# Optimization experiments

Measured on AMD Instinct MI355X. Metric: run time of the kernel, lower is better.

Reference implementation:

```python
import jax, jax.numpy as jnp
import numpy as np

B, N, F, H, F_ = 4, 2048, 64, 4, 64


def setup_inputs() -> dict:
    key = jax.random.key(0)
    kx, ka, kw, ks, kn = jax.random.split(key, 5)
    X = jax.random.normal(kx, (B, N, F), dtype=jnp.float32)
    A = (jax.random.uniform(ka, (B, N, N)) < 0.05).astype(jnp.float32)
    A = jnp.maximum(A, jnp.eye(N, dtype=jnp.float32)[None])
    W = jax.random.normal(kw, (H, F, F_), dtype=jnp.float32) * 0.1
    a_self = jax.random.normal(ks, (H, F_), dtype=jnp.float32) * 0.1
    a_neigh = jax.random.normal(kn, (H, F_), dtype=jnp.float32) * 0.1
    return {"X": X, "A": A, "W": W, "a_self": a_self, "a_neigh": a_neigh}


def reference(X, A, W, a_self, a_neigh):
    # linear transform per head: [B,H,N,F_]
    lin = jnp.einsum('bnf,hfo->bhno', X, W)
    # additive attention scores
    s_self = jnp.einsum('bhno,ho->bhn', lin, a_self)[:, :, :, None]   # [B,H,N,1]
    s_neigh = jnp.einsum('bhno,ho->bhn', lin, a_neigh)[:, :, None, :]  # [B,H,1,N]
    dense = s_self + s_neigh                                           # [B,H,N,N]
    dense = jnp.where(dense >= 0, dense, 0.2 * dense)                  # LeakyReLU(0.2)
    BIG = jnp.float32(1e10)
    mask = jnp.exp(A * -BIG) * -BIG                                    # 0 where edge, -1e10 where no edge
    logits = dense + mask[:, None, :, :]
    attn = jax.nn.softmax(logits, axis=-1)
    # dropout is identity at inference (attn_dropout=0.0)
    feats = jnp.einsum('bhnm,bhmo->bhno', attn, lin)                   # [B,H,N,F_]
    feats = jax.nn.relu(feats)                                         # activation before concat
    b, h, n, f_ = feats.shape
    out = feats.transpose(0, 2, 1, 3).reshape(b, n, h * f_)            # concat heads
    return out
```

## Files before the change

kernel.cpp:

```cpp
#include <hip/hip_runtime.h>
#include <hip/hip_bf16.h>

#define BB 4
#define NN 2048
#define FF 64
#define HH 4
#define FO 64
#define CAP 256


__global__ __launch_bounds__(256) void BatchGraphAttention_84378927497895_kernel(
    const float* __restrict__ W, const float* __restrict__ a_self,
    const float* __restrict__ a_neigh, float* __restrict__ w_self,
    float* __restrict__ w_neigh) {
  int t = threadIdx.x;
  int h = t >> 6;
  const float* Wp = W + t * FO;
  const float* as = a_self + h * FO;
  const float* an = a_neigh + h * FO;
  float acc_s = 0.f, acc_n = 0.f;
#pragma unroll
  for (int o = 0; o < FO; ++o) {
    float w = Wp[o];
    acc_s += w * as[o];
    acc_n += w * an[o];
  }
  w_self[t] = acc_s;
  w_neigh[t] = acc_n;
}

__global__ __launch_bounds__(256) void BatchGraphAttention_84378927497895_kernel2(
    const float* __restrict__ X, const float* __restrict__ w_self,
    const float* __restrict__ w_neigh, float* __restrict__ s_self,
    float* __restrict__ s_neigh) {
  int bn = blockIdx.x;
  int t = threadIdx.x, h = t >> 6, f = t & 63;
  float x = X[(size_t)bn * FF + f];
  float vs = x * w_self[h * FF + f];
  float vn = x * w_neigh[h * FF + f];
#pragma unroll
  for (int off = 32; off > 0; off >>= 1) {
    vs += __shfl_down(vs, off, 64);
    vn += __shfl_down(vn, off, 64);
  }
  if (f == 0) {
    int b = bn >> 11, n = bn & (NN - 1);
    int bh = b * HH + h;
    s_self[bh * NN + n] = vs;
    s_neigh[bh * NN + n] = vn;
  }
}

__global__ __launch_bounds__(256) void BatchGraphAttention_84378927497895_kernel3(
    const float* __restrict__ A, const float* __restrict__ X,
    const float* __restrict__ W, const float* __restrict__ s_self,
    const float* __restrict__ s_neigh, float* __restrict__ out) {
  int bn = blockIdx.x;
  int b = bn >> 11;
  int n = bn & (NN - 1);
  __shared__ unsigned short idx[CAP];
  __shared__ float plt[CAP][4];
  __shared__ float red[4][HH][FF];
  __shared__ float ys[HH][FF];
  __shared__ float sinv[HH];
  __shared__ int cnt_s;
  int t = threadIdx.x;
  int lane = t & 63, wv = t >> 6;
  if (t == 0) cnt_s = 0;
  __syncthreads();

  {
    const float4* Ar4 = (const float4*)(A + (size_t)bn * NN);
#pragma unroll
    for (int it = 0; it < 2; ++it) {
      int q = t + it * 256;
      float4 v = Ar4[q];
      unsigned base = (unsigned)q * 4u;
      if (v.x != 0.f) { int p = atomicAdd(&cnt_s, 1); if (p < CAP) idx[p] = (unsigned short)(base + 0); }
      if (v.y != 0.f) { int p = atomicAdd(&cnt_s, 1); if (p < CAP) idx[p] = (unsigned short)(base + 1); }
      if (v.z != 0.f) { int p = atomicAdd(&cnt_s, 1); if (p < CAP) idx[p] = (unsigned short)(base + 2); }
      if (v.w != 0.f) { int p = atomicAdd(&cnt_s, 1); if (p < CAP) idx[p] = (unsigned short)(base + 3); }
    }
  }
  __syncthreads();
  int cnt = cnt_s;
  if (cnt > CAP) cnt = CAP;

  {
    int h = wv;
    int bh = b * HH + h;
    float ss = s_self[bh * NN + n];
    const float* snp = s_neigh + (size_t)bh * NN;

    float lmax = -1e30f;
    for (int j = lane; j < cnt; j += 64) {
      float lg = ss + snp[idx[j]];
      lg = (lg >= 0.f) ? lg : 0.2f * lg;
      plt[j][h] = lg;
      lmax = fmaxf(lmax, lg);
    }
#pragma unroll
    for (int off = 32; off > 0; off >>= 1)
      lmax = fmaxf(lmax, __shfl_xor(lmax, off, 64));

    float lsum = 0.f;
    for (int j = lane; j < cnt; j += 64) {
      float e = __expf(plt[j][h] - lmax);
      plt[j][h] = e;
      lsum += e;
    }
#pragma unroll
    for (int off = 32; off > 0; off >>= 1) lsum += __shfl_xor(lsum, off, 64);
    if (lane == 0) sinv[h] = 1.f / lsum;
  }
  __syncthreads();

  {
    const float* xp = X + (size_t)b * NN * FF + lane;
    float y0 = 0.f, y1 = 0.f, y2 = 0.f, y3 = 0.f;
    int j = wv;
    for (; j + 12 < cnt; j += 16) {
      int m0 = idx[j], m1 = idx[j + 4], m2 = idx[j + 8], m3 = idx[j + 12];
      float4 p0 = *(const float4*)plt[j];
      float4 p1 = *(const float4*)plt[j + 4];
      float4 p2 = *(const float4*)plt[j + 8];
      float4 p3 = *(const float4*)plt[j + 12];
      float x0 = xp[m0 * FF];
      float x1 = xp[m1 * FF];
      float x2 = xp[m2 * FF];
      float x3 = xp[m3 * FF];
      y0 += p0.x * x0; y1 += p0.y * x0; y2 += p0.z * x0; y3 += p0.w * x0;
      y0 += p1.x * x1; y1 += p1.y * x1; y2 += p1.z * x1; y3 += p1.w * x1;
      y0 += p2.x * x2; y1 += p2.y * x2; y2 += p2.z * x2; y3 += p2.w * x2;
      y0 += p3.x * x3; y1 += p3.y * x3; y2 += p3.z * x3; y3 += p3.w * x3;
    }
    for (; j < cnt; j += 4) {
      float4 p = *(const float4*)plt[j];
      float x = xp[idx[j] * FF];
      y0 += p.x * x; y1 += p.y * x; y2 += p.z * x; y3 += p.w * x;
    }
    red[wv][0][lane] = y0;
    red[wv][1][lane] = y1;
    red[wv][2][lane] = y2;
    red[wv][3][lane] = y3;
  }
  __syncthreads();

  {
    int h = wv, f = lane;
    float s = red[0][h][f] + red[1][h][f] + red[2][h][f] + red[3][h][f];
    ys[h][f] = s * sinv[h];
  }
  __syncthreads();
  {
    const float* Wp = W + wv * FF * FO + lane;
    float acc = 0.f;
#pragma unroll
    for (int f = 0; f < FF; ++f) acc += ys[wv][f] * Wp[f * FO];
    acc = (acc > 0.f) ? acc : 0.f;
    out[(size_t)bn * (HH * FO) + t] = acc;
  }
}

extern "C" void kernel_launch(void* const* d_in, const int* in_sizes, int n_in,
                              void* d_out, int out_size, void* d_ws,
                              size_t ws_size, hipStream_t stream) {
  const float* X = (const float*)d_in[0];
  const float* A = (const float*)d_in[1];
  const float* W = (const float*)d_in[2];
  const float* a_self = (const float*)d_in[3];
  const float* a_neigh = (const float*)d_in[4];
  float* out = (float*)d_out;

  float* w_self = (float*)d_ws;
  float* w_neigh = w_self + HH * FF;
  float* s_self = w_neigh + HH * FF;
  float* s_neigh = s_self + (size_t)BB * HH * NN;

  BatchGraphAttention_84378927497895_kernel<<<1, 256, 0, stream>>>(
      W, a_self, a_neigh, w_self, w_neigh);
  BatchGraphAttention_84378927497895_kernel2<<<BB * NN, 256, 0, stream>>>(
      X, w_self, w_neigh, s_self, s_neigh);
  BatchGraphAttention_84378927497895_kernel3<<<BB * NN, 256, 0, stream>>>(
      A, X, W, s_self, s_neigh, out);
}
```

Measured before the change: 146.4 us.

## Process one node per wavefront with ballot compaction and head-interleaved scores

Both the score kernel and the attention kernel now map one graph node to each wavefront, four nodes per block, in place of one node per block. Neighbor compaction uses wave ballots and popcounts where it used LDS atomics. Scores are stored head-interleaved as float4 so one gather fetches all four heads. The output projection reuses each W load across the four nodes in the block. This drops most block barriers and the cross-wave reduction, and raises per-wave work and register use, so fewer waves are available to hide latency on the irregular X gathers.

```diff
diff --git a/kernel.cpp b/kernel.cpp
--- a/kernel.cpp
+++ b/kernel.cpp
@@ -1,5 +1,4 @@
 #include <hip/hip_runtime.h>
-#include <hip/hip_bf16.h>
 
 #define BB 4
 #define NN 2048
@@ -7,6 +6,8 @@
 #define HH 4
 #define FO 64
 #define CAP 256
+
+typedef unsigned short ushort_t;
 
 
 __global__ __launch_bounds__(256) void BatchGraphAttention_84378927497895_kernel(
@@ -31,135 +32,169 @@
 
 __global__ __launch_bounds__(256) void BatchGraphAttention_84378927497895_kernel2(
     const float* __restrict__ X, const float* __restrict__ w_self,
-    const float* __restrict__ w_neigh, float* __restrict__ s_self,
-    float* __restrict__ s_neigh) {
-  int bn = blockIdx.x;
-  int t = threadIdx.x, h = t >> 6, f = t & 63;
-  float x = X[(size_t)bn * FF + f];
-  float vs = x * w_self[h * FF + f];
-  float vn = x * w_neigh[h * FF + f];
-#pragma unroll
-  for (int off = 32; off > 0; off >>= 1) {
-    vs += __shfl_down(vs, off, 64);
-    vn += __shfl_down(vn, off, 64);
-  }
-  if (f == 0) {
-    int b = bn >> 11, n = bn & (NN - 1);
-    int bh = b * HH + h;
-    s_self[bh * NN + n] = vs;
-    s_neigh[bh * NN + n] = vn;
+    const float* __restrict__ w_neigh, float* __restrict__ s_self4,
+    float* __restrict__ s_neigh4) {
+  int t = threadIdx.x, lane = t & 63, wv = t >> 6;
+  int bn = blockIdx.x * 4 + wv;
+  int g = lane & 15;
+  int h = lane >> 4;
+  float4 x = ((const float4*)X)[(size_t)bn * 16 + g];
+  float4 ws = ((const float4*)w_self)[h * 16 + g];
+  float4 wn = ((const float4*)w_neigh)[h * 16 + g];
+  float vs = x.x * ws.x + x.y * ws.y + x.z * ws.z + x.w * ws.w;
+  float vn = x.x * wn.x + x.y * wn.y + x.z * wn.z + x.w * wn.w;
+#pragma unroll
+  for (int off = 1; off < 16; off <<= 1) {
+    vs += __shfl_xor(vs, off, 64);
+    vn += __shfl_xor(vn, off, 64);
+  }
+  if (g == 0) {
+    s_self4[bn * 4 + h] = vs;
+    s_neigh4[bn * 4 + h] = vn;
   }
 }
 
 __global__ __launch_bounds__(256) void BatchGraphAttention_84378927497895_kernel3(
     const float* __restrict__ A, const float* __restrict__ X,
-    const float* __restrict__ W, const float* __restrict__ s_self,
-    const float* __restrict__ s_neigh, float* __restrict__ out) {
-  int bn = blockIdx.x;
+    const float* __restrict__ W, const float* __restrict__ s_self4,
+    const float* __restrict__ s_neigh4, float* __restrict__ out) {
+  __shared__ float4 plt[4][CAP];
+  __shared__ ushort_t idxs[4][CAP];
+  int t = threadIdx.x, lane = t & 63, wv = t >> 6;
+  int bn = blockIdx.x * 4 + wv;
   int b = bn >> 11;
-  int n = bn & (NN - 1);
-  __shared__ unsigned short idx[CAP];
-  __shared__ float plt[CAP][4];
-  __shared__ float red[4][HH][FF];
-  __shared__ float ys[HH][FF];
-  __shared__ float sinv[HH];
-  __shared__ int cnt_s;
-  int t = threadIdx.x;
-  int lane = t & 63, wv = t >> 6;
-  if (t == 0) cnt_s = 0;
+  float4* pl = plt[wv];
+  ushort_t* idx = idxs[wv];
+
+  const float4* Ar = (const float4*)(A + (size_t)bn * NN);
+  float4 av[8];
+#pragma unroll
+  for (int r = 0; r < 8; ++r) av[r] = Ar[r * 64 + lane];
+  unsigned long long lt = (1ull << lane) - 1ull;
+  int cnt = 0;
+#pragma unroll
+  for (int r = 0; r < 8; ++r) {
+    unsigned c = (unsigned)((r * 64 + lane) * 4);
+    unsigned long long m0 = __ballot(av[r].x != 0.f);
+    if (av[r].x != 0.f) { int p = cnt + (int)__popcll(m0 & lt); if (p < CAP) idx[p] = (ushort_t)c; }
+    cnt += (int)__popcll(m0);
+    unsigned long long m1 = __ballot(av[r].y != 0.f);
+    if (av[r].y != 0.f) { int p = cnt + (int)__popcll(m1 & lt); if (p < CAP) idx[p] = (ushort_t)(c + 1); }
+    cnt += (int)__popcll(m1);
+    unsigned long long m2 = __ballot(av[r].z != 0.f);
+    if (av[r].z != 0.f) { int p = cnt + (int)__popcll(m2 & lt); if (p < CAP) idx[p] = (ushort_t)(c + 2); }
+    cnt += (int)__popcll(m2);
+    unsigned long long m3 = __ballot(av[r].w != 0.f);
+    if (av[r].w != 0.f) { int p = cnt + (int)__popcll(m3 & lt); if (p < CAP) idx[p] = (ushort_t)(c + 3); }
+    cnt += (int)__popcll(m3);
+  }
+  cnt = __builtin_amdgcn_readfirstlane(cnt);
+  if (cnt > CAP) cnt = CAP;
+
+  float4 ss = ((const float4*)s_self4)[bn];
+  const float4* sn = ((const float4*)s_neigh4) + (size_t)b * NN;
+  float4 lg0, lg1, lg2, lg3;
+  float4 lmax = make_float4(-3e38f, -3e38f, -3e38f, -3e38f);
+#define GAT_LOGIT(K, LG)                                                    \
+  {                                                                         \
+    int j = lane + K * 64;                                                  \
+    if (j < cnt) {                                                          \
+      int m = idx[j];                                                       \
+      float4 s = sn[m];                                                     \
+      LG.x = ss.x + s.x; LG.y = ss.y + s.y;                                 \
+      LG.z = ss.z + s.z; LG.w = ss.w + s.w;                                 \
+      LG.x = (LG.x >= 0.f) ? LG.x : 0.2f * LG.x;                            \
+      LG.y = (LG.y >= 0.f) ? LG.y : 0.2f * LG.y;                            \
+      LG.z = (LG.z >= 0.f) ? LG.z : 0.2f * LG.z;                            \
+      LG.w = (LG.w >= 0.f) ? LG.w : 0.2f * LG.w;                            \
+      lmax.x = fmaxf(lmax.x, LG.x); lmax.y = fmaxf(lmax.y, LG.y);           \
+      lmax.z = fmaxf(lmax.z, LG.z); lmax.w = fmaxf(lmax.w, LG.w);           \
+    }                                                                       \
+  }
+  GAT_LOGIT(0, lg0) GAT_LOGIT(1, lg1) GAT_LOGIT(2, lg2) GAT_LOGIT(3, lg3)
+#pragma unroll
+  for (int off = 1; off < 64; off <<= 1) {
+    lmax.x = fmaxf(lmax.x, __shfl_xor(lmax.x, off, 64));
+    lmax.y = fmaxf(lmax.y, __shfl_xor(lmax.y, off, 64));
+    lmax.z = fmaxf(lmax.z, __shfl_xor(lmax.z, off, 64));
+    lmax.w = fmaxf(lmax.w, __shfl_xor(lmax.w, off, 64));
+  }
+  float4 sum = make_float4(0.f, 0.f, 0.f, 0.f);
+#define EXP_STORE(K, LG)                                                    \
+  {                                                                         \
+    int j = lane + K * 64;                                                  \
+    if (j < cnt) {                                                          \
+      float4 e;                                                             \
+      e.x = __expf(LG.x - lmax.x); e.y = __expf(LG.y - lmax.y);             \
+      e.z = __expf(LG.z - lmax.z); e.w = __expf(LG.w - lmax.w);             \
+      sum.x += e.x; sum.y += e.y; sum.z += e.z; sum.w += e.w;               \
+      pl[j] = e;                                                            \
+    }                                                                       \
+  }
+  EXP_STORE(0, lg0) EXP_STORE(1, lg1) EXP_STORE(2, lg2) EXP_STORE(3, lg3)
+#pragma unroll
+  for (int off = 1; off < 64; off <<= 1) {
+    sum.x += __shfl_xor(sum.x, off, 64);
+    sum.y += __shfl_xor(sum.y, off, 64);
+    sum.z += __shfl_xor(sum.z, off, 64);
+    sum.w += __shfl_xor(sum.w, off, 64);
+  }
+  float4 sv;
+  sv.x = 1.f / sum.x; sv.y = 1.f / sum.y; sv.z = 1.f / sum.z; sv.w = 1.f / sum.w;
+
+  const float* xp = X + (size_t)b * (NN * FF) + lane;
+  float y0 = 0.f, y1 = 0.f, y2 = 0.f, y3 = 0.f;
+  int j = 0;
+  for (; j + 4 <= cnt; j += 4) {
+    uint2 pk = *(const uint2*)(idx + j);
+    float4 p0 = pl[j + 0];
+    float4 p1 = pl[j + 1];
+    float4 p2 = pl[j + 2];
+    float4 p3 = pl[j + 3];
+    int m0 = pk.x & 0xffff, m1 = pk.x >> 16;
+    int m2 = pk.y & 0xffff, m3 = pk.y >> 16;
+    float x0 = xp[m0 * FF];
+    float x1 = xp[m1 * FF];
+    float x2 = xp[m2 * FF];
+    float x3 = xp[m3 * FF];
+    y0 += p0.x * x0; y1 += p0.y * x0; y2 += p0.z * x0; y3 += p0.w * x0;
+    y0 += p1.x * x1; y1 += p1.y * x1; y2 += p1.z * x1; y3 += p1.w * x1;
+    y0 += p2.x * x2; y1 += p2.y * x2; y2 += p2.z * x2; y3 += p2.w * x2;
+    y0 += p3.x * x3; y1 += p3.y * x3; y2 += p3.z * x3; y3 += p3.w * x3;
+  }
+  for (; j < cnt; ++j) {
+    int m = idx[j];
+    float4 p = pl[j];
+    float x = xp[m * FF];
+    y0 += p.x * x; y1 += p.y * x; y2 += p.z * x; y3 += p.w * x;
+  }
+
+  pl[lane] = make_float4(y0 * sv.x, y1 * sv.y, y2 * sv.z, y3 * sv.w);
   __syncthreads();
 
   {
-    const float4* Ar4 = (const float4*)(A + (size_t)bn * NN);
-#pragma unroll
-    for (int it = 0; it < 2; ++it) {
-      int q = t + it * 256;
-      float4 v = Ar4[q];
-      unsigned base = (unsigned)q * 4u;
-      if (v.x != 0.f) { int p = atomicAdd(&cnt_s, 1); if (p < CAP) idx[p] = (unsigned short)(base + 0); }
-      if (v.y != 0.f) { int p = atomicAdd(&cnt_s, 1); if (p < CAP) idx[p] = (unsigned short)(base + 1); }
-      if (v.z != 0.f) { int p = atomicAdd(&cnt_s, 1); if (p < CAP) idx[p] = (unsigned short)(base + 2); }
-      if (v.w != 0.f) { int p = atomicAdd(&cnt_s, 1); if (p < CAP) idx[p] = (unsigned short)(base + 3); }
+    const float* Wh = W + wv * (FF * FO) + lane;
+    const float* y0p = (const float*)plt[0] + wv;
+    const float* y1p = (const float*)plt[1] + wv;
+    const float* y2p = (const float*)plt[2] + wv;
+    const float* y3p = (const float*)plt[3] + wv;
+    float b0 = 0.f, b1 = 0.f, b2 = 0.f, b3 = 0.f;
+#pragma unroll 8
+    for (int f = 0; f < FF; ++f) {
+      float wl = Wh[f * FO];
+      b0 += y0p[f * 4] * wl;
+      b1 += y1p[f * 4] * wl;
+      b2 += y2p[f * 4] * wl;
+      b3 += y3p[f * 4] * wl;
     }
-  }
-  __syncthreads();
-  int cnt = cnt_s;
-  if (cnt > CAP) cnt = CAP;
-
-  {
-    int h = wv;
-    int bh = b * HH + h;
-    float ss = s_self[bh * NN + n];
-    const float* snp = s_neigh + (size_t)bh * NN;
-
-    float lmax = -1e30f;
-    for (int j = lane; j < cnt; j += 64) {
-      float lg = ss + snp[idx[j]];
-      lg = (lg >= 0.f) ? lg : 0.2f * lg;
-      plt[j][h] = lg;
-      lmax = fmaxf(lmax, lg);
-    }
-#pragma unroll
-    for (int off = 32; off > 0; off >>= 1)
-      lmax = fmaxf(lmax, __shfl_xor(lmax, off, 64));
-
-    float lsum = 0.f;
-    for (int j = lane; j < cnt; j += 64) {
-      float e = __expf(plt[j][h] - lmax);
-      plt[j][h] = e;
-      lsum += e;
-    }
-#pragma unroll
-    for (int off = 32; off > 0; off >>= 1) lsum += __shfl_xor(lsum, off, 64);
-    if (lane == 0) sinv[h] = 1.f / lsum;
-  }
-  __syncthreads();
-
-  {
-    const float* xp = X + (size_t)b * NN * FF + lane;
-    float y0 = 0.f, y1 = 0.f, y2 = 0.f, y3 = 0.f;
-    int j = wv;
-    for (; j + 12 < cnt; j += 16) {
-      int m0 = idx[j], m1 = idx[j + 4], m2 = idx[j + 8], m3 = idx[j + 12];
-      float4 p0 = *(const float4*)plt[j];
-      float4 p1 = *(const float4*)plt[j + 4];
-      float4 p2 = *(const float4*)plt[j + 8];
-      float4 p3 = *(const float4*)plt[j + 12];
-      float x0 = xp[m0 * FF];
-      float x1 = xp[m1 * FF];
-      float x2 = xp[m2 * FF];
-      float x3 = xp[m3 * FF];
-      y0 += p0.x * x0; y1 += p0.y * x0; y2 += p0.z * x0; y3 += p0.w * x0;
-      y0 += p1.x * x1; y1 += p1.y * x1; y2 += p1.z * x1; y3 += p1.w * x1;
-      y0 += p2.x * x2; y1 += p2.y * x2; y2 += p2.z * x2; y3 += p2.w * x2;
-      y0 += p3.x * x3; y1 += p3.y * x3; y2 += p3.z * x3; y3 += p3.w * x3;
-    }
-    for (; j < cnt; j += 4) {
-      float4 p = *(const float4*)plt[j];
-      float x = xp[idx[j] * FF];
-      y0 += p.x * x; y1 += p.y * x; y2 += p.z * x; y3 += p.w * x;
-    }
-    red[wv][0][lane] = y0;
-    red[wv][1][lane] = y1;
-    red[wv][2][lane] = y2;
-    red[wv][3][lane] = y3;
-  }
-  __syncthreads();
-
-  {
-    int h = wv, f = lane;
-    float s = red[0][h][f] + red[1][h][f] + red[2][h][f] + red[3][h][f];
-    ys[h][f] = s * sinv[h];
-  }
-  __syncthreads();
-  {
-    const float* Wp = W + wv * FF * FO + lane;
-    float acc = 0.f;
-#pragma unroll
-    for (int f = 0; f < FF; ++f) acc += ys[wv][f] * Wp[f * FO];
-    acc = (acc > 0.f) ? acc : 0.f;
-    out[(size_t)bn * (HH * FO) + t] = acc;
-  }
+    size_t ob = (size_t)(blockIdx.x * 4) * (HH * FO) + wv * FO + lane;
+    out[ob + 0 * (HH * FO)] = fmaxf(b0, 0.f);
+    out[ob + 1 * (HH * FO)] = fmaxf(b1, 0.f);
+    out[ob + 2 * (HH * FO)] = fmaxf(b2, 0.f);
+    out[ob + 3 * (HH * FO)] = fmaxf(b3, 0.f);
+  }
+#undef GAT_LOGIT
+#undef EXP_STORE
 }
 
 extern "C" void kernel_launch(void* const* d_in, const int* in_sizes, int n_in,
@@ -174,13 +209,13 @@
 
   float* w_self = (float*)d_ws;
   float* w_neigh = w_self + HH * FF;
-  float* s_self = w_neigh + HH * FF;
-  float* s_neigh = s_self + (size_t)BB * HH * NN;
+  float* s_self4 = w_neigh + HH * FF;
+  float* s_neigh4 = s_self4 + (size_t)BB * NN * HH;
 
   BatchGraphAttention_84378927497895_kernel<<<1, 256, 0, stream>>>(
       W, a_self, a_neigh, w_self, w_neigh);
-  BatchGraphAttention_84378927497895_kernel2<<<BB * NN, 256, 0, stream>>>(
-      X, w_self, w_neigh, s_self, s_neigh);
-  BatchGraphAttention_84378927497895_kernel3<<<BB * NN, 256, 0, stream>>>(
-      A, X, W, s_self, s_neigh, out);
-}
+  BatchGraphAttention_84378927497895_kernel2<<<BB * NN / 4, 256, 0, stream>>>(
+      X, w_self, w_neigh, s_self4, s_neigh4);
+  BatchGraphAttention_84378927497895_kernel3<<<BB * NN / 4, 256, 0, stream>>>(
+      A, X, W, s_self4, s_neigh4, out);
+}
```

After: 134.0 us. -8.5%, faster.
